# Kernel tuning notes

Hardware: AMD Instinct MI355X
Metric: run time of the kernel (lower is better)

The kernel has to match this reference:

```python
import jax, jax.numpy as jnp
import numpy as np


def setup_inputs() -> dict:
    key = jax.random.key(0)
    ks = jax.random.split(key, 7)
    B, F, D = 1024, 32, 64
    H = [128, 128, 128]
    x = jax.random.normal(ks[0], (B, F, D), dtype=jnp.float32)
    # Conv1d(k=1) weights: (out, in) where in = prev_field * F, Kaiming-ish scale
    W0 = jax.random.normal(ks[1], (H[0], F * F), dtype=jnp.float32) * 0.02
    b0 = jnp.zeros((H[0],), dtype=jnp.float32)
    W1 = jax.random.normal(ks[2], (H[1], H[0] * F), dtype=jnp.float32) * 0.02
    b1 = jnp.zeros((H[1],), dtype=jnp.float32)
    W2 = jax.random.normal(ks[3], (H[2], H[1] * F), dtype=jnp.float32) * 0.02
    b2 = jnp.zeros((H[2],), dtype=jnp.float32)
    return {"x": x, "W0": W0, "b0": b0, "W1": W1, "b1": b1, "W2": W2, "b2": b2}


def reference(x, W0, b0, W1, b1, W2, b2):
    # CIN: per layer, outer product of current hidden with base fields along
    # embed dim, then 1x1 conv (channel mix) + ReLU. We fuse the bhmd
    # intermediate directly into the contraction: W reshaped to (o, h, m)
    # matches torch's reshape(b, h*m, d) channel ordering (h major, m minor).
    F = x.shape[1]
    x0 = x  # (b, m=F, d)
    h = x
    res = []
    for W, b in ((W0, b0), (W1, b1), (W2, b2)):
        o = W.shape[0]
        Wr = W.reshape(o, h.shape[1], F)  # (o, h, m)
        z = jnp.einsum('bhd,bmd,ohm->bod', h, x0, Wr) + b[None, :, None]
        h = jax.nn.relu(z)
        res.append(h)
    out = jnp.concatenate(res, axis=1)  # (b, sum(H), d)
    return jnp.sum(out, axis=-1)  # (b, sum(H))
```

## Files before the change

### kernel.cpp

```cpp
#include <hip/hip_runtime.h>
#include <stdint.h>


typedef __attribute__((ext_vector_type(8))) _Float16 f16x8;
typedef __attribute__((ext_vector_type(2))) _Float16 f16x2;
typedef __attribute__((ext_vector_type(4))) float f32x4;
typedef __attribute__((ext_vector_type(4))) int i32x4;

union AB {
  i32x4 i;
  f16x8 h;
  uint32_t u[4];
};

static __device__ __forceinline__ uint32_t pkmul(uint32_t a, uint32_t b) {
  f16x2 r = __builtin_bit_cast(f16x2, a) * __builtin_bit_cast(f16x2, b);
  return __builtin_bit_cast(uint32_t, r);
}
static __device__ __forceinline__ uint32_t pkcvt(float a, float b) {
  return __builtin_bit_cast(uint32_t, __builtin_amdgcn_cvt_pkrtz(a, b));
}

#define HP 136

__global__ __launch_bounds__(512, 6) void cin_main(
    const float* __restrict__ x, const uint16_t* __restrict__ wp,
    const float* __restrict__ bias0, const float* __restrict__ bias1,
    const float* __restrict__ bias2, float* __restrict__ out) {
  __shared__ __align__(16) uint16_t hT[64][HP];

  const int tid = threadIdx.x;
  const int w = tid >> 6, lane = tid & 63;
  const int q = lane >> 4;
  const int i = lane & 15;
  const int b = blockIdx.x;

  for (int e = tid; e < 2048; e += 512) {
    int m = e >> 6, d = e & 63;
    hT[d][m] =
        __builtin_bit_cast(uint16_t, (_Float16)x[(size_t)b * 2048 + m * 64 + d]);
  }
  __syncthreads();

  AB xf[4];
#pragma unroll
  for (int t = 0; t < 4; ++t)
    xf[t].i = *(const i32x4*)&hT[t * 16 + i][q * 8];

  f32x4 acc[4];

#pragma unroll
  for (int L = 0; L < 3; ++L) {
    const int Kch = (L == 0) ? 32 : 128;
    const uint16_t* wl = (L == 0) ? wp : (L == 1) ? wp + 131072 : wp + 655360;
    const float* bias = (L == 0) ? bias0 : (L == 1) ? bias1 : bias2;

    const uint16_t* wptr = wl + (size_t)w * Kch * 512 + lane * 8;

#pragma unroll
    for (int t = 0; t < 4; ++t) acc[t] = (f32x4){0.f, 0.f, 0.f, 0.f};

    AB wbuf[2][2];
    uint32_t hvA[4], hvB[4];

    auto loadSlot = [&](int s, int c) {
      int cw = (c < Kch) ? c : 0;
#pragma unroll
      for (int cc = 0; cc < 2; ++cc)
        wbuf[s][cc].i = *(const i32x4*)(wptr + (size_t)(cw + cc) * 512);
    };
    auto loadHv = [&](uint32_t (&hv)[4], int c) {
      int cw = (c < Kch) ? c : 0;
#pragma unroll
      for (int t = 0; t < 4; ++t)
        hv[t] = *(const uint32_t*)&hT[t * 16 + i][cw];
    };
    auto computePair = [&](const AB (&wb)[2], const uint32_t (&hv)[4]) {
#pragma unroll
      for (int cc = 0; cc < 2; ++cc)
#pragma unroll
        for (int t = 0; t < 4; ++t) {
          uint32_t hd = __builtin_amdgcn_perm(hv[t], hv[t],
                                              cc ? 0x03020302u : 0x01000100u);
          AB bf;
#pragma unroll
          for (int k = 0; k < 4; ++k) bf.u[k] = pkmul(hd, xf[t].u[k]);
          acc[t] = __builtin_amdgcn_mfma_f32_16x16x32_f16(wb[cc].h, bf.h,
                                                          acc[t], 0, 0, 0);
        }
    };

    loadSlot(0, 0);
    loadSlot(1, 2);
    loadHv(hvA, 0);

#pragma unroll 1
    for (int c0 = 0; c0 < Kch; c0 += 4) {
      loadHv(hvB, c0 + 2);
      computePair(wbuf[0], hvA);
      loadSlot(0, c0 + 4);
      __builtin_amdgcn_sched_barrier(0);
      loadHv(hvA, c0 + 4);
      computePair(wbuf[1], hvB);
      loadSlot(1, c0 + 6);
      __builtin_amdgcn_sched_barrier(0);
    }

    f32x4 bv = *(const f32x4*)(bias + w * 16 + q * 4);
#pragma unroll
    for (int t = 0; t < 4; ++t)
#pragma unroll
      for (int r = 0; r < 4; ++r)
        acc[t][r] = fmaxf(acc[t][r] + bv[r], 0.f);

    if (L < 2) {
      __syncthreads();
#pragma unroll
      for (int t = 0; t < 4; ++t) {
        uint2 pk;
        pk.x = pkcvt(acc[t][0], acc[t][1]);
        pk.y = pkcvt(acc[t][2], acc[t][3]);
        *(uint2*)&hT[t * 16 + i][w * 16 + q * 4] = pk;
      }
    }

#pragma unroll
    for (int r = 0; r < 4; ++r) {
      float s = acc[0][r] + acc[1][r] + acc[2][r] + acc[3][r];
      s += __shfl_xor(s, 1);
      s += __shfl_xor(s, 2);
      s += __shfl_xor(s, 4);
      s += __shfl_xor(s, 8);
      if (i == 0)
        out[(size_t)b * 384 + L * 128 + w * 16 + q * 4 + r] = s;
    }

    if (L < 2) __syncthreads();
  }
}

__global__ void pack_w_all(const float* __restrict__ W0, const float* __restrict__ W1,
                           const float* __restrict__ W2, uint16_t* __restrict__ Wp) {
  int blk = blockIdx.x;
  const float* W;
  uint16_t* dst;
  int kshift;
  if (blk < 64)       { W = W0; dst = Wp;          kshift = 5; }
  else if (blk < 320) { W = W1; dst = Wp + 131072; kshift = 7; blk -= 64; }
  else                { W = W2; dst = Wp + 655360; kshift = 7; blk -= 320; }
  int idx = blk * 256 + threadIdx.x;
  int Kq = 1 << (kshift + 2);
  int o = idx >> (kshift + 2);
  int kq = idx & (Kq - 1);
  int c = kq >> 2, q = kq & 3;
  int ot = o >> 4, ii = o & 15;
  const float* src = W + ((size_t)o << (kshift + 5)) + kq * 8;
  uint4 val;
  val.x = pkcvt(src[0], src[1]);
  val.y = pkcvt(src[2], src[3]);
  val.z = pkcvt(src[4], src[5]);
  val.w = pkcvt(src[6], src[7]);
  *(uint4*)(dst + ((((size_t)ot << kshift) + c) << 9) + (q << 7) + (ii << 3)) = val;
}

extern "C" void kernel_launch(void* const* d_in, const int* in_sizes, int n_in,
                              void* d_out, int out_size, void* d_ws, size_t ws_size,
                              hipStream_t stream) {
  (void)in_sizes; (void)n_in; (void)out_size; (void)ws_size;
  const float* x  = (const float*)d_in[0];
  const float* W0 = (const float*)d_in[1];
  const float* b0 = (const float*)d_in[2];
  const float* W1 = (const float*)d_in[3];
  const float* b1 = (const float*)d_in[4];
  const float* W2 = (const float*)d_in[5];
  const float* b2 = (const float*)d_in[6];
  uint16_t* wpacked = (uint16_t*)d_ws;

  hipLaunchKernelGGL(pack_w_all, dim3(576), dim3(256), 0, stream, W0, W1, W2, wpacked);
  hipLaunchKernelGGL(cin_main, dim3(1024), dim3(512), 0, stream,
                     x, wpacked, b0, b1, b2, (float*)d_out);
}
```

Baseline: 233.0 us.

## Switch to 32x32x16 MFMA tiles with 4 waves per block

Replaces the 16x16x32 MFMA tiling (8 waves, 16 output channels each) with 32x32x16 MFMA tiles where each of 4 waves owns 32 output channels and two 32-wide d-tiles. The weight packing layout, LDS fragment loads, epilogue and reduction are all remapped to the 32x32 accumulator layout. The aim is to halve weight-fragment loads per FLOP and cut the elementwise outer-product (pkmul) work per MFMA. In exchange it gives fewer waves per block and larger accumulator register pressure, which may reduce latency hiding.

```diff
diff --git a/kernel.cpp b/kernel.cpp
--- a/kernel.cpp
+++ b/kernel.cpp
@@ -5,6 +5,7 @@
 typedef __attribute__((ext_vector_type(8))) _Float16 f16x8;
 typedef __attribute__((ext_vector_type(2))) _Float16 f16x2;
 typedef __attribute__((ext_vector_type(4))) float f32x4;
+typedef __attribute__((ext_vector_type(16))) float f32x16;
 typedef __attribute__((ext_vector_type(4))) int i32x4;
 
 union AB {
@@ -23,31 +24,33 @@
 
 #define HP 136
 
-__global__ __launch_bounds__(512, 6) void cin_main(
+__global__ __launch_bounds__(256, 4) void cin_main(
     const float* __restrict__ x, const uint16_t* __restrict__ wp,
     const float* __restrict__ bias0, const float* __restrict__ bias1,
     const float* __restrict__ bias2, float* __restrict__ out) {
   __shared__ __align__(16) uint16_t hT[64][HP];
 
   const int tid = threadIdx.x;
-  const int w = tid >> 6, lane = tid & 63;
-  const int q = lane >> 4;
-  const int i = lane & 15;
+  const int ot = tid >> 6, lane = tid & 63;
+  const int hi = lane >> 5;
+  const int l31 = lane & 31;
   const int b = blockIdx.x;
 
-  for (int e = tid; e < 2048; e += 512) {
+  for (int e = tid; e < 2048; e += 256) {
     int m = e >> 6, d = e & 63;
     hT[d][m] =
         __builtin_bit_cast(uint16_t, (_Float16)x[(size_t)b * 2048 + m * 64 + d]);
   }
   __syncthreads();
 
-  AB xf[4];
-#pragma unroll
-  for (int t = 0; t < 4; ++t)
-    xf[t].i = *(const i32x4*)&hT[t * 16 + i][q * 8];
-
-  f32x4 acc[4];
+  AB xf[2][2];
+#pragma unroll
+  for (int dt = 0; dt < 2; ++dt)
+#pragma unroll
+    for (int s = 0; s < 2; ++s)
+      xf[dt][s].i = *(const i32x4*)&hT[dt * 32 + l31][s * 16 + hi * 8];
+
+  f32x16 acc0, acc1;
 
 #pragma unroll
   for (int L = 0; L < 3; ++L) {
@@ -55,39 +58,50 @@
     const uint16_t* wl = (L == 0) ? wp : (L == 1) ? wp + 131072 : wp + 655360;
     const float* bias = (L == 0) ? bias0 : (L == 1) ? bias1 : bias2;
 
-    const uint16_t* wptr = wl + (size_t)w * Kch * 512 + lane * 8;
-
-#pragma unroll
-    for (int t = 0; t < 4; ++t) acc[t] = (f32x4){0.f, 0.f, 0.f, 0.f};
-
-    AB wbuf[2][2];
-    uint32_t hvA[4], hvB[4];
-
-    auto loadSlot = [&](int s, int c) {
+    const uint16_t* wptr = wl + (size_t)ot * Kch * 1024 + lane * 8;
+
+#pragma unroll
+    for (int r = 0; r < 16; ++r) { acc0[r] = 0.f; acc1[r] = 0.f; }
+
+    AB wbuf[2][4];
+    uint32_t hvA[2], hvB[2];
+
+    auto loadSlot = [&](int sl, int c) {
       int cw = (c < Kch) ? c : 0;
 #pragma unroll
       for (int cc = 0; cc < 2; ++cc)
-        wbuf[s][cc].i = *(const i32x4*)(wptr + (size_t)(cw + cc) * 512);
+#pragma unroll
+        for (int s = 0; s < 2; ++s)
+          wbuf[sl][cc * 2 + s].i =
+              *(const i32x4*)(wptr + (size_t)(cw + cc) * 1024 + s * 512);
     };
-    auto loadHv = [&](uint32_t (&hv)[4], int c) {
+    auto loadHv = [&](uint32_t (&hv)[2], int c) {
       int cw = (c < Kch) ? c : 0;
 #pragma unroll
-      for (int t = 0; t < 4; ++t)
-        hv[t] = *(const uint32_t*)&hT[t * 16 + i][cw];
+      for (int dt = 0; dt < 2; ++dt)
+        hv[dt] = *(const uint32_t*)&hT[dt * 32 + l31][cw];
     };
-    auto computePair = [&](const AB (&wb)[2], const uint32_t (&hv)[4]) {
-#pragma unroll
-      for (int cc = 0; cc < 2; ++cc)
-#pragma unroll
-        for (int t = 0; t < 4; ++t) {
-          uint32_t hd = __builtin_amdgcn_perm(hv[t], hv[t],
-                                              cc ? 0x03020302u : 0x01000100u);
-          AB bf;
-#pragma unroll
-          for (int k = 0; k < 4; ++k) bf.u[k] = pkmul(hd, xf[t].u[k]);
-          acc[t] = __builtin_amdgcn_mfma_f32_16x16x32_f16(wb[cc].h, bf.h,
-                                                          acc[t], 0, 0, 0);
+    auto computeStep = [&](const AB (&wb)[4], const uint32_t (&hv)[2]) {
+#pragma unroll
+      for (int cc = 0; cc < 2; ++cc) {
+        uint32_t hd0 = __builtin_amdgcn_perm(hv[0], hv[0],
+                                             cc ? 0x03020302u : 0x01000100u);
+        uint32_t hd1 = __builtin_amdgcn_perm(hv[1], hv[1],
+                                             cc ? 0x03020302u : 0x01000100u);
+#pragma unroll
+        for (int s = 0; s < 2; ++s) {
+          AB bf0, bf1;
+#pragma unroll
+          for (int k = 0; k < 4; ++k) {
+            bf0.u[k] = pkmul(hd0, xf[0][s].u[k]);
+            bf1.u[k] = pkmul(hd1, xf[1][s].u[k]);
+          }
+          acc0 = __builtin_amdgcn_mfma_f32_32x32x16_f16(wb[cc * 2 + s].h,
+                                                        bf0.h, acc0, 0, 0, 0);
+          acc1 = __builtin_amdgcn_mfma_f32_32x32x16_f16(wb[cc * 2 + s].h,
+                                                        bf1.h, acc1, 0, 0, 0);
         }
+      }
     };
 
     loadSlot(0, 0);
@@ -97,42 +111,55 @@
 #pragma unroll 1
     for (int c0 = 0; c0 < Kch; c0 += 4) {
       loadHv(hvB, c0 + 2);
-      computePair(wbuf[0], hvA);
+      computeStep(wbuf[0], hvA);
       loadSlot(0, c0 + 4);
       __builtin_amdgcn_sched_barrier(0);
       loadHv(hvA, c0 + 4);
-      computePair(wbuf[1], hvB);
+      computeStep(wbuf[1], hvB);
       loadSlot(1, c0 + 6);
       __builtin_amdgcn_sched_barrier(0);
     }
 
-    f32x4 bv = *(const f32x4*)(bias + w * 16 + q * 4);
-#pragma unroll
-    for (int t = 0; t < 4; ++t)
-#pragma unroll
-      for (int r = 0; r < 4; ++r)
-        acc[t][r] = fmaxf(acc[t][r] + bv[r], 0.f);
+    f32x4 bv[4];
+#pragma unroll
+    for (int rg = 0; rg < 4; ++rg)
+      bv[rg] = *(const f32x4*)(bias + ot * 32 + 8 * rg + 4 * hi);
+#pragma unroll
+    for (int r = 0; r < 16; ++r) {
+      acc0[r] = fmaxf(acc0[r] + bv[r >> 2][r & 3], 0.f);
+      acc1[r] = fmaxf(acc1[r] + bv[r >> 2][r & 3], 0.f);
+    }
 
     if (L < 2) {
       __syncthreads();
 #pragma unroll
-      for (int t = 0; t < 4; ++t) {
-        uint2 pk;
-        pk.x = pkcvt(acc[t][0], acc[t][1]);
-        pk.y = pkcvt(acc[t][2], acc[t][3]);
-        *(uint2*)&hT[t * 16 + i][w * 16 + q * 4] = pk;
+      for (int rg = 0; rg < 4; ++rg) {
+        uint2 pk0, pk1;
+        pk0.x = pkcvt(acc0[4 * rg + 0], acc0[4 * rg + 1]);
+        pk0.y = pkcvt(acc0[4 * rg + 2], acc0[4 * rg + 3]);
+        pk1.x = pkcvt(acc1[4 * rg + 0], acc1[4 * rg + 1]);
+        pk1.y = pkcvt(acc1[4 * rg + 2], acc1[4 * rg + 3]);
+        int ch = ot * 32 + 8 * rg + 4 * hi;
+        *(uint2*)&hT[l31][ch] = pk0;
+        *(uint2*)&hT[32 + l31][ch] = pk1;
       }
     }
 
 #pragma unroll
-    for (int r = 0; r < 4; ++r) {
-      float s = acc[0][r] + acc[1][r] + acc[2][r] + acc[3][r];
-      s += __shfl_xor(s, 1);
-      s += __shfl_xor(s, 2);
-      s += __shfl_xor(s, 4);
-      s += __shfl_xor(s, 8);
-      if (i == 0)
-        out[(size_t)b * 384 + L * 128 + w * 16 + q * 4 + r] = s;
+    for (int rg = 0; rg < 4; ++rg) {
+      f32x4 s4;
+#pragma unroll
+      for (int rr = 0; rr < 4; ++rr) {
+        float s = acc0[4 * rg + rr] + acc1[4 * rg + rr];
+        s += __shfl_xor(s, 1);
+        s += __shfl_xor(s, 2);
+        s += __shfl_xor(s, 4);
+        s += __shfl_xor(s, 8);
+        s += __shfl_xor(s, 16);
+        s4[rr] = s;
+      }
+      if (l31 == 0)
+        *(f32x4*)(out + (size_t)b * 384 + L * 128 + ot * 32 + 8 * rg + 4 * hi) = s4;
     }
 
     if (L < 2) __syncthreads();
@@ -152,15 +179,16 @@
   int Kq = 1 << (kshift + 2);
   int o = idx >> (kshift + 2);
   int kq = idx & (Kq - 1);
-  int c = kq >> 2, q = kq & 3;
-  int ot = o >> 4, ii = o & 15;
+  int c = kq >> 2, s = (kq >> 1) & 1, hi = kq & 1;
+  int ot = o >> 5, li = o & 31;
   const float* src = W + ((size_t)o << (kshift + 5)) + kq * 8;
   uint4 val;
   val.x = pkcvt(src[0], src[1]);
   val.y = pkcvt(src[2], src[3]);
   val.z = pkcvt(src[4], src[5]);
   val.w = pkcvt(src[6], src[7]);
-  *(uint4*)(dst + ((((size_t)ot << kshift) + c) << 9) + (q << 7) + (ii << 3)) = val;
+  size_t d16 = ((((size_t)(ot << kshift) + c) * 2 + s) << 9) + (hi << 8) + (li << 3);
+  *(uint4*)(dst + d16) = val;
 }
 
 extern "C" void kernel_launch(void* const* d_in, const int* in_sizes, int n_in,
@@ -177,6 +205,6 @@
   uint16_t* wpacked = (uint16_t*)d_ws;
 
   hipLaunchKernelGGL(pack_w_all, dim3(576), dim3(256), 0, stream, W0, W1, W2, wpacked);
-  hipLaunchKernelGGL(cin_main, dim3(1024), dim3(512), 0, stream,
+  hipLaunchKernelGGL(cin_main, dim3(1024), dim3(256), 0, stream,
                      x, wpacked, b0, b1, b2, (float*)d_out);
 }
```

Result: faster. 214.8 us (-7.8%).
